# Kernel optimization log

Measured on AMD Instinct MI355X. Metric: run time of the kernel, lower is better.

The kernel has to match this reference:

```python
import jax, jax.numpy as jnp
import numpy as np

NR = 2048
NS_PLUS_NU = 80
ALPHA = 0.6      # leak rate
SIGMA_B = 1.6    # additive bias
SIGMA = 0.084    # input matrix scale
RHO_SR = 0.8     # spectral-radius scale (approximated for the random dense A)


def setup_inputs() -> dict:
    key = jax.random.key(0)
    k1, k2, k3, k4 = jax.random.split(key, 4)
    batch, seq_len = 32, 1024
    inp = jax.random.normal(k1, (batch, seq_len, NS_PLUS_NU), dtype=jnp.float32)
    r_0 = jax.random.normal(k2, (1, batch, NR), dtype=jnp.float32)
    # Reservoir matrix A: sparse uniform(-1,1), scaled to spectral radius rho_sr.
    # For the reference we use a dense random matrix scaled so its spectral radius
    # is ~rho_sr (circular law: sr of uniform(-1,1)/sqrt(3) NxN ~ sqrt(N/3)).
    A = jax.random.uniform(k3, (NR, NR), dtype=jnp.float32, minval=-1.0, maxval=1.0)
    A = A * (RHO_SR / jnp.sqrt(NR / 3.0))
    # Input matrix B: uniform(-sigma, sigma), shape (Nr, Ns+Nu)
    B = jax.random.uniform(k4, (NR, NS_PLUS_NU), dtype=jnp.float32, minval=-SIGMA, maxval=SIGMA)
    return {"input": inp, "r_0": r_0, "A": A, "B": B}


def reference(input, r_0, A, B):
    # Precompute input projection for all timesteps: (batch, seq, Nr)
    bu = jnp.einsum('bsu,ru->bsr', input, B) + SIGMA_B
    bu_t = jnp.swapaxes(bu, 0, 1)  # (seq, batch, Nr) for scan

    def step(r, bu_s):
        r_new = (1.0 - ALPHA) * r + ALPHA * jnp.tanh(r @ A.T + bu_s)
        return r_new, r_new

    r_final, res = jax.lax.scan(step, r_0[0], bu_t)
    reservoir = jnp.swapaxes(res, 0, 1)  # (batch, seq, Nr)
    return reservoir, r_final[None]  # (batch, seq, Nr), (1, batch, Nr)
```

## Files before the change

kernel.cpp:

```cpp
#include <hip/hip_runtime.h>
#include <cmath>

typedef _Float16 f16;
typedef _Float16 f16x8 __attribute__((ext_vector_type(8)));
typedef float f32x4 __attribute__((ext_vector_type(4)));

#define NR 2048
#define NU 80
#define NUP 96
#define NB 32
#define NS 1024
#define NWG 64
#define ALPHA 0.6f
#define SIGMA_B 1.6f

#define FLAG_STRIDE 16
#define FLAGS_BYTES (NWG * FLAG_STRIDE * 4)

#define OFF_AF   0ull
#define OFF_XP   (OFF_AF  + (size_t)NR*NR*2)
#define OFF_BP   (OFF_XP  + (size_t)NS*NB*NUP*2)
#define OFF_RB0  (OFF_BP  + (size_t)NR*NUP*2)
#define OFF_RB1  (OFF_RB0 + (size_t)NB*NR*2)
#define OFF_FLG  (OFF_RB1 + (size_t)NB*NR*2)

__global__ void prep_kernel(const float* __restrict__ input,
                            const float* __restrict__ r0,
                            const float* __restrict__ A,
                            const float* __restrict__ B,
                            f16* __restrict__ Af, f16* __restrict__ xp,
                            f16* __restrict__ Bp, f16* __restrict__ rb0)
{
    const int stride = gridDim.x * blockDim.x;
    const int tid = blockIdx.x * blockDim.x + threadIdx.x;
    for (int i = tid; i < NR * NR; i += stride) Af[i] = (f16)A[i];
    for (int i = tid; i < NS * NB * NUP; i += stride) {
        int u = i % NUP; int sb = i / NUP; int b = sb % NB; int s = sb / NB;
        xp[i] = (u < NU) ? (f16)input[((size_t)b * NS + s) * NU + u] : (f16)0.0f;
    }
    for (int i = tid; i < NR * NUP; i += stride) {
        int u = i % NUP; int j = i / NUP;
        Bp[i] = (u < NU) ? (f16)B[j * NU + u] : (f16)0.0f;
    }
    for (int i = tid; i < NB * NR; i += stride) rb0[i] = (f16)r0[i];
}

#define MFMA(va, vb, vc) __builtin_amdgcn_mfma_f32_16x16x32_f16(va, vb, vc, 0, 0, 0)

__global__ __launch_bounds__(256, 1) void scan_kernel(
    float* __restrict__ out,
    const float* __restrict__ r0,
    const f16* __restrict__ Af, const f16* __restrict__ xp,
    const f16* __restrict__ Bp, f16* __restrict__ rb0a, f16* __restrict__ rb1a,
    int* __restrict__ flags)
{
    const int tid  = threadIdx.x;
    const int lane = tid & 63;
    const int kq   = tid >> 6;
    const int cg   = blockIdx.x;
    const int rt   = kq >> 1;
    const int ct   = kq & 1;

    const int fr = lane & 15;
    const int kg = lane >> 4;

    __shared__ f32x4 lds_part[4][4][64];
    __shared__ f16   lds_r[32 * 36];

    f16x8 bf[2][16];
    #pragma unroll
    for (int c = 0; c < 2; ++c) {
        const f16* base = Af + (size_t)(cg * 32 + c * 16 + fr) * NR + kq * 512 + kg * 8;
        #pragma unroll
        for (int kk = 0; kk < 16; ++kk)
            bf[c][kk] = *(const f16x8*)(base + kk * 32);
    }
    #pragma unroll
    for (int c = 0; c < 2; ++c)
        #pragma unroll
        for (int kk = 0; kk < 16; ++kk)
            asm volatile("" : "+v"(bf[c][kk]));

    f16x8 bp[2][3];
    if (kq == 3) {
        #pragma unroll
        for (int c = 0; c < 2; ++c) {
            const f16* base = Bp + (size_t)(cg * 32 + c * 16 + fr) * NUP + kg * 8;
            #pragma unroll
            for (int k2 = 0; k2 < 3; ++k2) {
                bp[c][k2] = *(const f16x8*)(base + k2 * 32);
                asm volatile("" : "+v"(bp[c][k2]));
            }
        }
    }

    float rm[4];
    #pragma unroll
    for (int i = 0; i < 4; ++i)
        rm[i] = r0[(size_t)(rt * 16 + kg * 4 + i) * NR + cg * 32 + ct * 16 + fr];

    f16* rcur = rb0a;
    f16* rnxt = rb1a;
    int* myflag = flags + (size_t)cg * FLAG_STRIDE;
    int* pollp  = flags + (size_t)(kq * 16 + (lane & 15)) * FLAG_STRIDE;

    for (int s = 0; s < NS; ++s) {
        f16x8 q0, q1, q2, q3, q4, q5;
        if (kq == 3) {
            const f16* xb0 = xp + ((size_t)s * NB + fr) * NUP + kg * 8;
            q0 = *(const f16x8*)(xb0);
            q1 = *(const f16x8*)(xb0 + 32);
            q2 = *(const f16x8*)(xb0 + 64);
            const f16* xb1 = xb0 + 16 * NUP;
            q3 = *(const f16x8*)(xb1);
            q4 = *(const f16x8*)(xb1 + 32);
            q5 = *(const f16x8*)(xb1 + 64);
        }
        if (s) {
            const int tgt = s;
            while (true) {
                int v = 0x7fffffff;
                if (lane < 16)
                    v = __hip_atomic_load(pollp, __ATOMIC_RELAXED,
                                          __HIP_MEMORY_SCOPE_AGENT);
                if (__all(v >= tgt)) break;
                __builtin_amdgcn_s_sleep(1);
            }
        }

        f32x4 a00 = {0,0,0,0}, a01 = {0,0,0,0}, a10 = {0,0,0,0}, a11 = {0,0,0,0};
        if (kq == 3) {
            a00 = MFMA(q0, bp[0][0], a00); a01 = MFMA(q0, bp[1][0], a01);
            a10 = MFMA(q3, bp[0][0], a10); a11 = MFMA(q3, bp[1][0], a11);
            a00 = MFMA(q1, bp[0][1], a00); a01 = MFMA(q1, bp[1][1], a01);
            a10 = MFMA(q4, bp[0][1], a10); a11 = MFMA(q4, bp[1][1], a11);
            a00 = MFMA(q2, bp[0][2], a00); a01 = MFMA(q2, bp[1][2], a01);
            a10 = MFMA(q5, bp[0][2], a10); a11 = MFMA(q5, bp[1][2], a11);
        }

        const f16* rp0 = rcur + (size_t)fr * NR + kq * 512 + kg * 8;
        const f16* rp1 = rp0 + 16 * NR;
        f16x8 x[32];
        #define LDX(j) asm volatile("global_load_dwordx4 %0, %1, off offset:%2 sc0 sc1" \
            : "=v"(x[j]) : "v"(((j) & 1) ? rp1 : rp0), "n"(((j) >> 1) * 64) : "memory")
        #define MFG(kk) \
            a00 = MFMA(x[2*(kk)],   bf[0][kk], a00); \
            a01 = MFMA(x[2*(kk)],   bf[1][kk], a01); \
            a10 = MFMA(x[2*(kk)+1], bf[0][kk], a10); \
            a11 = MFMA(x[2*(kk)+1], bf[1][kk], a11);
        #define WAITV(n) asm volatile("s_waitcnt vmcnt(" #n ")" ::: "memory"); \
            __builtin_amdgcn_sched_barrier(0)

        LDX(0);  LDX(1);  LDX(2);  LDX(3);  LDX(4);  LDX(5);  LDX(6);  LDX(7);
        LDX(8);  LDX(9);  LDX(10); LDX(11); LDX(12); LDX(13); LDX(14); LDX(15);
        WAITV(8);
        MFG(0); MFG(1); MFG(2); MFG(3);
        __builtin_amdgcn_sched_barrier(0);
        LDX(16); LDX(17); LDX(18); LDX(19); LDX(20); LDX(21); LDX(22); LDX(23);
        WAITV(8);
        MFG(4); MFG(5); MFG(6); MFG(7);
        __builtin_amdgcn_sched_barrier(0);
        LDX(24); LDX(25); LDX(26); LDX(27); LDX(28); LDX(29); LDX(30); LDX(31);
        WAITV(8);
        MFG(8); MFG(9); MFG(10); MFG(11);
        WAITV(0);
        MFG(12); MFG(13); MFG(14); MFG(15);
        #undef LDX
        #undef MFG
        #undef WAITV

        lds_part[kq][0][lane] = a00;
        lds_part[kq][1][lane] = a01;
        lds_part[kq][2][lane] = a10;
        lds_part[kq][3][lane] = a11;
        __syncthreads();

        const int tile = kq;
        f32x4 sum = lds_part[0][tile][lane] + lds_part[1][tile][lane]
                  + lds_part[2][tile][lane] + lds_part[3][tile][lane];

        float rn[4];
        #pragma unroll
        for (int i = 0; i < 4; ++i) {
            float sval = sum[i] + SIGMA_B;
            float v = (1.0f - ALPHA) * rm[i] + ALPHA * tanhf(sval);
            rm[i] = v;
            rn[i] = v;
            lds_r[(rt * 16 + kg * 4 + i) * 36 + ct * 16 + fr] = (f16)v;
        }
        __syncthreads();

        if (s != NS - 1) {
            int row = tid >> 3, seg = tid & 7;
            unsigned long long v = *(const unsigned long long*)&lds_r[row * 36 + seg * 4];
            asm volatile("global_store_dwordx2 %0, %1, off sc0 sc1"
                         :: "v"(rnxt + (size_t)row * NR + cg * 32 + seg * 4), "v"(v)
                         : "memory");
            asm volatile("s_waitcnt vmcnt(0)" ::: "memory");
            __syncthreads();
            if (tid == 0)
                __hip_atomic_store(myflag, s + 1, __ATOMIC_RELAXED,
                                   __HIP_MEMORY_SCOPE_AGENT);
        }

        #pragma unroll
        for (int i = 0; i < 4; ++i)
            __builtin_nontemporal_store(rn[i],
                out + ((size_t)(rt * 16 + kg * 4 + i) * NS + s) * NR
                    + cg * 32 + ct * 16 + fr);

        f16* t = rcur; rcur = rnxt; rnxt = t;
    }

    #pragma unroll
    for (int i = 0; i < 4; ++i)
        out[(size_t)NB * NS * NR
            + (size_t)(rt * 16 + kg * 4 + i) * NR + cg * 32 + ct * 16 + fr] = rm[i];
}

extern "C" void kernel_launch(void* const* d_in, const int* in_sizes, int n_in,
                              void* d_out, int out_size, void* d_ws, size_t ws_size,
                              hipStream_t stream)
{
    const float* input = (const float*)d_in[0];
    const float* r0    = (const float*)d_in[1];
    const float* A     = (const float*)d_in[2];
    const float* B     = (const float*)d_in[3];
    float* out = (float*)d_out;
    char* ws = (char*)d_ws;

    f16* Af  = (f16*)(ws + OFF_AF);
    f16* xp  = (f16*)(ws + OFF_XP);
    f16* Bp  = (f16*)(ws + OFF_BP);
    f16* rb0 = (f16*)(ws + OFF_RB0);
    f16* rb1 = (f16*)(ws + OFF_RB1);
    int* flg = (int*)(ws + OFF_FLG);

    hipMemsetAsync(flg, 0, FLAGS_BYTES, stream);
    prep_kernel<<<2048, 256, 0, stream>>>(input, r0, A, B, Af, xp, Bp, rb0);
    scan_kernel<<<NWG, 256, 0, stream>>>(out, r0, Af, xp, Bp, rb0, rb1, flg);
}
```

Baseline: 6.022 ms.

## Replace flag-based step sync with parity tags embedded in fp16 state LSBs

Removes the per-workgroup flag array and its store-wait-barrier-flag sequence. The low mantissa bit of each fp16 reservoir value now carries a step-parity tag. Consumers poll the data itself and re-read their whole tile until every tag matches. This cuts one global round trip and one barrier per step. In exchange it loses one bit of fp16 precision, re-loads the tile on a mismatch, and uses bounded spins that can fall through silently if the wait runs too long.

```diff
diff --git a/kernel.cpp b/kernel.cpp
--- a/kernel.cpp
+++ b/kernel.cpp
@@ -4,6 +4,7 @@
 typedef _Float16 f16;
 typedef _Float16 f16x8 __attribute__((ext_vector_type(8)));
 typedef float f32x4 __attribute__((ext_vector_type(4)));
+typedef unsigned long long u64;
 
 #define NR 2048
 #define NU 80
@@ -13,23 +14,22 @@
 #define NWG 64
 #define ALPHA 0.6f
 #define SIGMA_B 1.6f
-
-#define FLAG_STRIDE 16
-#define FLAGS_BYTES (NWG * FLAG_STRIDE * 4)
+#define POLL_BOUND (1 << 20)
+#define RETRY_BOUND 4096
 
 #define OFF_AF   0ull
-#define OFF_XP   (OFF_AF  + (size_t)NR*NR*2)
-#define OFF_BP   (OFF_XP  + (size_t)NS*NB*NUP*2)
-#define OFF_RB0  (OFF_BP  + (size_t)NR*NUP*2)
-#define OFF_RB1  (OFF_RB0 + (size_t)NB*NR*2)
-#define OFF_FLG  (OFF_RB1 + (size_t)NB*NR*2)
+#define OFF_XP   (OFF_AF + (size_t)NR*NR*2)
+#define OFF_BP   (OFF_XP + (size_t)NS*NB*NUP*2)
+#define OFF_RB   (OFF_BP + (size_t)NR*NUP*2)
+
+__device__ __host__ inline int tag_of_step(int s) { return (((s >> 1) + 1) & 1); }
 
 __global__ void prep_kernel(const float* __restrict__ input,
                             const float* __restrict__ r0,
                             const float* __restrict__ A,
                             const float* __restrict__ B,
                             f16* __restrict__ Af, f16* __restrict__ xp,
-                            f16* __restrict__ Bp, f16* __restrict__ rb0)
+                            f16* __restrict__ Bp, f16* __restrict__ rb)
 {
     const int stride = gridDim.x * blockDim.x;
     const int tid = blockIdx.x * blockDim.x + threadIdx.x;
@@ -42,17 +42,28 @@
         int u = i % NUP; int j = i / NUP;
         Bp[i] = (u < NU) ? (f16)B[j * NU + u] : (f16)0.0f;
     }
-    for (int i = tid; i < NB * NR; i += stride) rb0[i] = (f16)r0[i];
+    for (int i = tid; i < NB * NR; i += stride) {
+        f16 h = (f16)r0[i];
+        unsigned short b = __builtin_bit_cast(unsigned short, h);
+        b = (unsigned short)((b & ~1u) | 1u);
+        rb[i] = __builtin_bit_cast(f16, b);
+    }
 }
 
 #define MFMA(va, vb, vc) __builtin_amdgcn_mfma_f32_16x16x32_f16(va, vb, vc, 0, 0, 0)
+
+__device__ inline f16x8 pack16(u64 lo, u64 hi) {
+    u64 t[2] = { lo, hi };
+    f16x8 r;
+    __builtin_memcpy(&r, t, 16);
+    return r;
+}
 
 __global__ __launch_bounds__(256, 1) void scan_kernel(
     float* __restrict__ out,
     const float* __restrict__ r0,
     const f16* __restrict__ Af, const f16* __restrict__ xp,
-    const f16* __restrict__ Bp, f16* __restrict__ rb0a, f16* __restrict__ rb1a,
-    int* __restrict__ flags)
+    const f16* __restrict__ Bp, f16* __restrict__ rbuf)
 {
     const int tid  = threadIdx.x;
     const int lane = tid & 63;
@@ -60,12 +71,11 @@
     const int cg   = blockIdx.x;
     const int rt   = kq >> 1;
     const int ct   = kq & 1;
-
-    const int fr = lane & 15;
-    const int kg = lane >> 4;
+    const int fr   = lane & 15;
+    const int kg   = lane >> 4;
 
     __shared__ f32x4 lds_part[4][4][64];
-    __shared__ f16   lds_r[32 * 36];
+    __shared__ f16   lds_r[32 * 40];
 
     f16x8 bf[2][16];
     #pragma unroll
@@ -99,33 +109,61 @@
     for (int i = 0; i < 4; ++i)
         rm[i] = r0[(size_t)(rt * 16 + kg * 4 + i) * NR + cg * 32 + ct * 16 + fr];
 
-    f16* rcur = rb0a;
-    f16* rnxt = rb1a;
-    int* myflag = flags + (size_t)cg * FLAG_STRIDE;
-    int* pollp  = flags + (size_t)(kq * 16 + (lane & 15)) * FLAG_STRIDE;
-
     for (int s = 0; s < NS; ++s) {
+        const f16* cur = rbuf + (size_t)(s & 1) * NB * NR;
+        f16*       nxt = rbuf + (size_t)((s + 1) & 1) * NB * NR;
+        const int  tc  = tag_of_step(s);
+        const int  tn  = tag_of_step(s + 1);
+        const u64  tmask = 0x0001000100010001ull;
+        const u64  texp  = tc ? tmask : 0ull;
+
         f16x8 q0, q1, q2, q3, q4, q5;
         if (kq == 3) {
             const f16* xb0 = xp + ((size_t)s * NB + fr) * NUP + kg * 8;
+            const f16* xb1 = xb0 + 16 * NUP;
             q0 = *(const f16x8*)(xb0);
             q1 = *(const f16x8*)(xb0 + 32);
             q2 = *(const f16x8*)(xb0 + 64);
-            const f16* xb1 = xb0 + 16 * NUP;
             q3 = *(const f16x8*)(xb1);
             q4 = *(const f16x8*)(xb1 + 32);
             q5 = *(const f16x8*)(xb1 + 64);
         }
+
         if (s) {
-            const int tgt = s;
+            const int* pc = (const int*)(cur + kq * 512 + (lane & 15) * 32);
+            int spins = 0;
             while (true) {
-                int v = 0x7fffffff;
+                int w = tc;
                 if (lane < 16)
-                    v = __hip_atomic_load(pollp, __ATOMIC_RELAXED,
-                                          __HIP_MEMORY_SCOPE_AGENT);
-                if (__all(v >= tgt)) break;
-                __builtin_amdgcn_s_sleep(1);
+                    w = __hip_atomic_load(pc, __ATOMIC_RELAXED,
+                                          __HIP_MEMORY_SCOPE_AGENT) & 1;
+                if (__all(w == tc)) break;
+                if (++spins > POLL_BOUND) break;
+                __builtin_amdgcn_s_sleep(2);
             }
+        }
+
+        u64 xv[64];
+        int retry = 0;
+        while (true) {
+            #pragma unroll
+            for (int kk = 0; kk < 16; ++kk) {
+                #pragma unroll
+                for (int rtl = 0; rtl < 2; ++rtl) {
+                    const u64* p = (const u64*)(cur
+                        + (size_t)(fr + 16 * rtl) * NR + kq * 512 + kk * 32 + kg * 8);
+                    xv[kk * 4 + rtl * 2 + 0] =
+                        __hip_atomic_load(p, __ATOMIC_RELAXED, __HIP_MEMORY_SCOPE_AGENT);
+                    xv[kk * 4 + rtl * 2 + 1] =
+                        __hip_atomic_load(p + 1, __ATOMIC_RELAXED, __HIP_MEMORY_SCOPE_AGENT);
+                }
+            }
+            u64 bad = 0;
+            #pragma unroll
+            for (int i = 0; i < 64; ++i) bad |= (xv[i] ^ texp) & tmask;
+            if (__all(bad == 0ull)) break;
+            if (++retry > RETRY_BOUND) break;
+            __builtin_amdgcn_s_sleep(2);
         }
 
         f32x4 a00 = {0,0,0,0}, a01 = {0,0,0,0}, a10 = {0,0,0,0}, a11 = {0,0,0,0};
@@ -137,37 +175,13 @@
             a00 = MFMA(q2, bp[0][2], a00); a01 = MFMA(q2, bp[1][2], a01);
             a10 = MFMA(q5, bp[0][2], a10); a11 = MFMA(q5, bp[1][2], a11);
         }
-
-        const f16* rp0 = rcur + (size_t)fr * NR + kq * 512 + kg * 8;
-        const f16* rp1 = rp0 + 16 * NR;
-        f16x8 x[32];
-        #define LDX(j) asm volatile("global_load_dwordx4 %0, %1, off offset:%2 sc0 sc1" \
-            : "=v"(x[j]) : "v"(((j) & 1) ? rp1 : rp0), "n"(((j) >> 1) * 64) : "memory")
-        #define MFG(kk) \
-            a00 = MFMA(x[2*(kk)],   bf[0][kk], a00); \
-            a01 = MFMA(x[2*(kk)],   bf[1][kk], a01); \
-            a10 = MFMA(x[2*(kk)+1], bf[0][kk], a10); \
-            a11 = MFMA(x[2*(kk)+1], bf[1][kk], a11);
-        #define WAITV(n) asm volatile("s_waitcnt vmcnt(" #n ")" ::: "memory"); \
-            __builtin_amdgcn_sched_barrier(0)
-
-        LDX(0);  LDX(1);  LDX(2);  LDX(3);  LDX(4);  LDX(5);  LDX(6);  LDX(7);
-        LDX(8);  LDX(9);  LDX(10); LDX(11); LDX(12); LDX(13); LDX(14); LDX(15);
-        WAITV(8);
-        MFG(0); MFG(1); MFG(2); MFG(3);
-        __builtin_amdgcn_sched_barrier(0);
-        LDX(16); LDX(17); LDX(18); LDX(19); LDX(20); LDX(21); LDX(22); LDX(23);
-        WAITV(8);
-        MFG(4); MFG(5); MFG(6); MFG(7);
-        __builtin_amdgcn_sched_barrier(0);
-        LDX(24); LDX(25); LDX(26); LDX(27); LDX(28); LDX(29); LDX(30); LDX(31);
-        WAITV(8);
-        MFG(8); MFG(9); MFG(10); MFG(11);
-        WAITV(0);
-        MFG(12); MFG(13); MFG(14); MFG(15);
-        #undef LDX
-        #undef MFG
-        #undef WAITV
+        #pragma unroll
+        for (int kk = 0; kk < 16; ++kk) {
+            f16x8 x0 = pack16(xv[kk * 4 + 0], xv[kk * 4 + 1]);
+            f16x8 x1 = pack16(xv[kk * 4 + 2], xv[kk * 4 + 3]);
+            a00 = MFMA(x0, bf[0][kk], a00); a01 = MFMA(x0, bf[1][kk], a01);
+            a10 = MFMA(x1, bf[0][kk], a10); a11 = MFMA(x1, bf[1][kk], a11);
+        }
 
         lds_part[kq][0][lane] = a00;
         lds_part[kq][1][lane] = a01;
@@ -182,34 +196,33 @@
         float rn[4];
         #pragma unroll
         for (int i = 0; i < 4; ++i) {
-            float sval = sum[i] + SIGMA_B;
-            float v = (1.0f - ALPHA) * rm[i] + ALPHA * tanhf(sval);
+            float v = (1.0f - ALPHA) * rm[i] + ALPHA * tanhf(sum[i] + SIGMA_B);
             rm[i] = v;
             rn[i] = v;
-            lds_r[(rt * 16 + kg * 4 + i) * 36 + ct * 16 + fr] = (f16)v;
+            f16 h = (f16)v;
+            unsigned short b = __builtin_bit_cast(unsigned short, h);
+            b = (unsigned short)((b & ~1u) | (unsigned)tn);
+            lds_r[(rt * 16 + kg * 4 + i) * 40 + ct * 16 + fr] = __builtin_bit_cast(f16, b);
         }
         __syncthreads();
 
-        if (s != NS - 1) {
-            int row = tid >> 3, seg = tid & 7;
-            unsigned long long v = *(const unsigned long long*)&lds_r[row * 36 + seg * 4];
-            asm volatile("global_store_dwordx2 %0, %1, off sc0 sc1"
-                         :: "v"(rnxt + (size_t)row * NR + cg * 32 + seg * 4), "v"(v)
-                         : "memory");
-            asm volatile("s_waitcnt vmcnt(0)" ::: "memory");
-            __syncthreads();
-            if (tid == 0)
-                __hip_atomic_store(myflag, s + 1, __ATOMIC_RELAXED,
-                                   __HIP_MEMORY_SCOPE_AGENT);
-        }
-
-        #pragma unroll
-        for (int i = 0; i < 4; ++i)
-            __builtin_nontemporal_store(rn[i],
-                out + ((size_t)(rt * 16 + kg * 4 + i) * NS + s) * NR
-                    + cg * 32 + ct * 16 + fr);
-
-        f16* t = rcur; rcur = rnxt; rnxt = t;
+        if (s != NS - 1 && tid < 128) {
+            int row = tid >> 2, seg = tid & 3;
+            const u64* lp = (const u64*)&lds_r[row * 40 + seg * 8];
+            u64 v0 = lp[0], v1 = lp[1];
+            u64* pp = (u64*)(nxt + (size_t)row * NR + cg * 32 + seg * 8);
+            __hip_atomic_store(pp,     v0, __ATOMIC_RELAXED, __HIP_MEMORY_SCOPE_AGENT);
+            __hip_atomic_store(pp + 1, v1, __ATOMIC_RELAXED, __HIP_MEMORY_SCOPE_AGENT);
+        }
+
+        {
+            float* po = out + ((size_t)(rt * 16 + kg * 4) * NS + s) * NR
+                        + cg * 32 + ct * 16 + fr;
+            __builtin_nontemporal_store(rn[0], po + 0ull * NS * NR);
+            __builtin_nontemporal_store(rn[1], po + 1ull * NS * NR);
+            __builtin_nontemporal_store(rn[2], po + 2ull * NS * NR);
+            __builtin_nontemporal_store(rn[3], po + 3ull * NS * NR);
+        }
     }
 
     #pragma unroll
@@ -229,14 +242,11 @@
     float* out = (float*)d_out;
     char* ws = (char*)d_ws;
 
-    f16* Af  = (f16*)(ws + OFF_AF);
-    f16* xp  = (f16*)(ws + OFF_XP);
-    f16* Bp  = (f16*)(ws + OFF_BP);
-    f16* rb0 = (f16*)(ws + OFF_RB0);
-    f16* rb1 = (f16*)(ws + OFF_RB1);
-    int* flg = (int*)(ws + OFF_FLG);
-
-    hipMemsetAsync(flg, 0, FLAGS_BYTES, stream);
-    prep_kernel<<<2048, 256, 0, stream>>>(input, r0, A, B, Af, xp, Bp, rb0);
-    scan_kernel<<<NWG, 256, 0, stream>>>(out, r0, Af, xp, Bp, rb0, rb1, flg);
-}
+    f16* Af = (f16*)(ws + OFF_AF);
+    f16* xp = (f16*)(ws + OFF_XP);
+    f16* Bp = (f16*)(ws + OFF_BP);
+    f16* rb = (f16*)(ws + OFF_RB);
+
+    prep_kernel<<<2048, 256, 0, stream>>>(input, r0, A, B, Af, xp, Bp, rb);
+    scan_kernel<<<NWG, 256, 0, stream>>>(out, r0, Af, xp, Bp, rb);
+}
```

Result: slower. 9.599 ms (+59.4%).
